# Optimization experiments

Hardware: AMD Instinct MI355X
Metric: run time of the kernel (lower is better)

## Reference

```python
import jax, jax.numpy as jnp
import numpy as np

NUM_USER = 50000
NUM_ITEM = 50000
NUM_NODES = NUM_USER + NUM_ITEM
DIM_LATENT = 256
DIM_ID = 64
NUM_EDGES = 2_000_000


def setup_inputs() -> dict:
    key = jax.random.key(0)
    ks = jax.random.split(key, 16)
    xn = lambda k, shape, s: (jax.random.normal(k, shape, dtype=jnp.float32) * s)
    # xavier-normal-ish std for [in,out] weights
    def xavier(k, fan_in, fan_out):
        std = float(np.sqrt(2.0 / (fan_in + fan_out)))
        return jax.random.normal(k, (fan_in, fan_out), dtype=jnp.float32) * std
    edge_index = jax.random.randint(ks[0], (2, NUM_EDGES), 0, NUM_NODES, dtype=jnp.int64)
    return {
        "features": xn(ks[1], (NUM_ITEM, DIM_LATENT), 1.0),
        "id_embedding": xn(ks[2], (NUM_NODES, DIM_ID), 1.0),
        "preference": xn(ks[3], (NUM_USER, DIM_LATENT), 0.1),
        "W_gcn0": xavier(ks[4], DIM_LATENT, DIM_ID),
        "W_gcn1": xavier(ks[5], DIM_ID, DIM_ID),
        "lin_w0": xavier(ks[6], DIM_LATENT, DIM_ID),
        "lin_b0": jnp.zeros((DIM_ID,), jnp.float32),
        "lin_w1": xavier(ks[7], DIM_ID, DIM_ID),
        "lin_b1": jnp.zeros((DIM_ID,), jnp.float32),
        "g_w0": xavier(ks[8], DIM_ID, DIM_ID),
        "g_b0": jnp.zeros((DIM_ID,), jnp.float32),
        "g_w1": xavier(ks[9], DIM_ID, DIM_ID),
        "g_b1": jnp.zeros((DIM_ID,), jnp.float32),
        "edge_index": edge_index,
    }


def _gcn(x, W, row, col, norm):
    # H = scatter_add(row, (x W)[col] * norm)
    h = x @ W                                  # [N, out]
    msg = h[col] * norm[:, None]               # [E, out] gather + scale
    return jax.ops.segment_sum(msg, row, num_segments=NUM_NODES)


def reference(features, id_embedding, preference, W_gcn0, W_gcn1,
              lin_w0, lin_b0, lin_w1, lin_b1, g_w0, g_b0, g_w1, g_b1,
              edge_index):
    row, col = edge_index[0], edge_index[1]
    # degree normalization: deg from scatter_add of ones over row
    deg = jax.ops.segment_sum(jnp.ones((row.shape[0],), jnp.float32), row,
                              num_segments=NUM_NODES)
    deg = jnp.maximum(deg, 1.0)
    dis = deg ** -0.5
    norm = dis[row] * dis[col]                 # [E]

    x = jnp.concatenate([preference, features], axis=0)   # [N, dim_latent]
    x = x / jnp.maximum(jnp.linalg.norm(x, axis=1, keepdims=True), 1e-12)

    lrelu = jax.nn.leaky_relu  # slope 0.01, matches torch default
    for W_gcn, lin_w, lin_b, g_w, g_b in (
        (W_gcn0, lin_w0, lin_b0, g_w0, g_b0),
        (W_gcn1, lin_w1, lin_b1, g_w1, g_b1),
    ):
        h = lrelu(_gcn(x, W_gcn, row, col, norm))          # [N, dim_id]
        x_hat = lrelu(x @ lin_w + lin_b) + id_embedding    # has_id=True
        x = lrelu(h @ g_w + g_b + x_hat)                   # concate=False
    return x
```

## Files before the change

### kernel.cpp

```cpp
#include <hip/hip_runtime.h>

#define NUM_USER   50000
#define NUM_ITEM   50000
#define NUM_NODES  100000
#define DIM_LATENT 256
#define DIM_ID     64
#define NUM_EDGES  2000000
#define NBUCKET    391
#define BPB        4096
#define NCHUNK     489
#define HSTRIDE    392
#define MAXBKT     8192
#define ZROW       NUM_NODES

typedef __attribute__((ext_vector_type(8))) short bf8_t;
typedef __attribute__((ext_vector_type(4))) float f4_t;
typedef __attribute__((ext_vector_type(2))) float f2_t;

static __device__ __forceinline__ float lrelu(float x) {
    return x > 0.0f ? x : 0.01f * x;
}
static __device__ __forceinline__ unsigned short f2bf(float f) {
    unsigned u = __float_as_uint(f);
    u += 0x7fff + ((u >> 16) & 1);
    return (unsigned short)(u >> 16);
}
static __device__ __forceinline__ unsigned cvtpk_bf16(float lo, float hi) {
    unsigned r;
    asm("v_cvt_pk_bf16_f32 %0, %1, %2" : "=v"(r) : "v"(lo), "v"(hi));
    return r;
}
static __device__ __forceinline__ float bf2f(unsigned short u) {
    return __uint_as_float(((unsigned)u) << 16);
}
static __device__ __forceinline__ float bflo(unsigned u) {
    return __uint_as_float(u << 16);
}
static __device__ __forceinline__ float bfhi(unsigned u) {
    return __uint_as_float(u & 0xffff0000u);
}
static __device__ __forceinline__ f2_t shfl2(f2_t v, int off) {
    long long l = __shfl_xor(__builtin_bit_cast(long long, v), off);
    return __builtin_bit_cast(f2_t, l);
}

__global__ void __launch_bounds__(256) k_hist(const int* __restrict__ row,
                                              int* __restrict__ hist) {
    __shared__ int lh[NBUCKET];
    const int g = blockIdx.x, t = threadIdx.x;
    for (int i = t; i < NBUCKET; i += 256) lh[i] = 0;
    __syncthreads();
    const int base = g * BPB;
    for (int i = 0; i < BPB; i += 256) {
        int e = base + i + t;
        if (e < NUM_EDGES) atomicAdd(&lh[row[e] >> 8], 1);
    }
    __syncthreads();
    for (int i = t; i < NBUCKET; i += 256) hist[g * HSTRIDE + i] = lh[i];
}

__global__ void __launch_bounds__(512) k_off1(int* __restrict__ hist,
                                              int* __restrict__ bcnt) {
    __shared__ int wsum[8];
    const int b = blockIdx.x, t = threadIdx.x;
    const int lane = t & 63, w = t >> 6;
    int c = (t < NCHUNK) ? hist[t * HSTRIDE + b] : 0;
    int v = c;
    #pragma unroll
    for (int off = 1; off < 64; off <<= 1) {
        int u = __shfl_up(v, off);
        if (lane >= off) v += u;
    }
    if (lane == 63) wsum[w] = v;
    __syncthreads();
    int add = 0;
    #pragma unroll
    for (int i = 0; i < 8; ++i) if (i < w) add += wsum[i];
    int incl = v + add;
    if (t < NCHUNK) hist[t * HSTRIDE + b] = incl - c;
    if (t == 511) bcnt[b] = incl;
}

__global__ void __launch_bounds__(512) k_bscan(const int* __restrict__ bcnt,
                                               int* __restrict__ boff) {
    __shared__ int wsum[8];
    const int t = threadIdx.x;
    const int lane = t & 63, w = t >> 6;
    int c = (t < NBUCKET) ? bcnt[t] : 0;
    int v = c;
    #pragma unroll
    for (int off = 1; off < 64; off <<= 1) {
        int u = __shfl_up(v, off);
        if (lane >= off) v += u;
    }
    if (lane == 63) wsum[w] = v;
    __syncthreads();
    int add = 0;
    #pragma unroll
    for (int i = 0; i < 8; ++i) if (i < w) add += wsum[i];
    int ex = v + add - c;
    if (t < NBUCKET) boff[t] = ex;
    if (t == NBUCKET - 1) boff[NBUCKET] = ex + c;
}

__global__ void __launch_bounds__(256) k_bin2(const int* __restrict__ row,
                                              const int* __restrict__ col,
                                              const int* __restrict__ hist,
                                              const int* __restrict__ boff,
                                              unsigned* __restrict__ epk) {
    __shared__ int curs[NBUCKET];
    const int g = blockIdx.x, t = threadIdx.x;
    for (int i = t; i < NBUCKET; i += 256) curs[i] = boff[i] + hist[g * HSTRIDE + i];
    __syncthreads();
    const int base = g * BPB;
    for (int i = 0; i < BPB; i += 256) {
        int e = base + i + t;
        if (e < NUM_EDGES) {
            int r = row[e];
            int pos = atomicAdd(&curs[r >> 8], 1);
            epk[pos] = ((unsigned)(r & 255) << 24) | (unsigned)col[e];
        }
    }
}

__global__ void __launch_bounds__(512) k_csr(unsigned* __restrict__ epk,
                                             const int* __restrict__ boff,
                                             int* __restrict__ offs,
                                             int* __restrict__ cnt,
                                             float* __restrict__ dis) {
    __shared__ unsigned stage[MAXBKT];
    __shared__ int lcnt[256];
    __shared__ int lofs[256];
    __shared__ int wsum[4];
    const int b = blockIdx.x, t = threadIdx.x;
    const int start = boff[b];
    int m = boff[b + 1] - start;
    if (m > MAXBKT) m = MAXBKT;

    if (t < 256) lcnt[t] = 0;
    for (int e = t; e < m; e += 512) stage[e] = epk[start + e];
    __syncthreads();
    for (int e = t; e < m; e += 512) atomicAdd(&lcnt[stage[e] >> 24], 1);
    __syncthreads();

    const int lane = t & 63, w = t >> 6;
    int c = (t < 256) ? lcnt[t] : 0;
    int v = c;
    #pragma unroll
    for (int off = 1; off < 64; off <<= 1) {
        int u = __shfl_up(v, off);
        if (lane >= off) v += u;
    }
    if (t < 256 && lane == 63) wsum[w] = v;
    __syncthreads();
    if (t < 256) {
        int add = 0;
        #pragma unroll
        for (int i = 0; i < 4; ++i) if (i < w) add += wsum[i];
        int ex = v + add - c;
        lofs[t] = start + ex;
        int n = (b << 8) + t;
        if (n < NUM_NODES) {
            offs[n] = start + ex;
            cnt[n]  = c;
            dis[n]  = rsqrtf((float)max(c, 1));
        }
    }
    __syncthreads();
    for (int e = t; e < m; e += 512) {
        unsigned p = stage[e];
        int pos = atomicAdd(&lofs[p >> 24], 1);
        epk[pos] = p & 0x00ffffffu;
    }
}

__global__ void __launch_bounds__(256) k_wprep(const float* __restrict__ Wg,
                                               const float* __restrict__ Wl,
                                               unsigned short* __restrict__ wfrag,
                                               unsigned* __restrict__ hbf8z) {
    if (blockIdx.x == 0 && threadIdx.x < 16)
        hbf8z[(size_t)ZROW * 16 + threadIdx.x] = 0u;
    int g = blockIdx.x * 256 + threadIdx.x;
    if (g >= 4096) return;
    int ks = g >> 9;
    int t  = (g >> 6) & 7;
    int l  = g & 63;
    const float* W = (t < 4) ? Wg : Wl;
    int colg = (t & 3) * 16 + (l & 15);
    int kb = ks * 32 + (l >> 4) * 8;
    unsigned short o[8];
    #pragma unroll
    for (int e = 0; e < 8; ++e) o[e] = f2bf(W[(size_t)(kb + e) * DIM_ID + colg]);
    unsigned short* dst = wfrag + (size_t)g * 8;
    #pragma unroll
    for (int e = 0; e < 8; ++e) dst[e] = o[e];
}

__global__ void __launch_bounds__(256) k_wprep64(const float* __restrict__ W0,
                                                 const float* __restrict__ W1,
                                                 const float* __restrict__ W2,
                                                 const float* __restrict__ W3,
                                                 unsigned short* __restrict__ frag) {
    int g = blockIdx.x * 256 + threadIdx.x;
    if (g >= 2048) return;
    int m = g >> 9;
    int r = g & 511;
    int ks = r >> 8;
    int t  = (r >> 6) & 3;
    int l  = r & 63;
    const float* W = (m == 0) ? W0 : (m == 1) ? W1 : (m == 2) ? W2 : W3;
    int colg = t * 16 + (l & 15);
    int kb = ks * 32 + (l >> 4) * 8;
    unsigned short o[8];
    #pragma unroll
    for (int e = 0; e < 8; ++e) o[e] = f2bf(W[(size_t)(kb + e) * DIM_ID + colg]);
    unsigned short* dst = frag + (size_t)g * 8;
    #pragma unroll
    for (int e = 0; e < 8; ++e) dst[e] = o[e];
}

__global__ void __launch_bounds__(256, 3) k_l1(
    const float* __restrict__ pref, const float* __restrict__ feat,
    const unsigned short* __restrict__ wfrag,
    const float* __restrict__ lb,   const float* __restrict__ idemb,
    const float* __restrict__ dis,
    unsigned char* __restrict__ hbf8, unsigned short* __restrict__ xhat)
{
    __shared__ unsigned short st[4][16][68];
    const int lane = threadIdx.x & 63;
    const int w = threadIdx.x >> 6;
    const int ql = lane & 15, q = lane >> 4;
    const int rowBase = (blockIdx.x * 4 + w) * 16;
    const int rown = rowBase + ql;
    const int rc = (rown < NUM_NODES) ? rown : 0;
    const float* src = (rc < NUM_USER) ? (pref + (size_t)rc * DIM_LATENT)
                                       : (feat + (size_t)(rc - NUM_USER) * DIM_LATENT);

    bf8_t af[8];
    float ss = 0.0f;
    #pragma unroll
    for (int ks = 0; ks < 8; ++ks) {
        float4 va = *reinterpret_cast<const float4*>(src + ks * 32 + q * 8);
        float4 vb = *reinterpret_cast<const float4*>(src + ks * 32 + q * 8 + 4);
        ss += va.x*va.x + va.y*va.y + va.z*va.z + va.w*va.w
            + vb.x*vb.x + vb.y*vb.y + vb.z*vb.z + vb.w*vb.w;
        uint4 au;
        au.x = cvtpk_bf16(va.x, va.y);
        au.y = cvtpk_bf16(va.z, va.w);
        au.z = cvtpk_bf16(vb.x, vb.y);
        au.w = cvtpk_bf16(vb.z, vb.w);
        af[ks] = __builtin_bit_cast(bf8_t, au);
    }
    ss += __shfl_xor(ss, 16);
    ss += __shfl_xor(ss, 32);
    float rn = 1.0f / fmaxf(sqrtf(ss), 1e-12f);

    f4_t acc[8];
    #pragma unroll
    for (int t = 0; t < 8; ++t) acc[t] = (f4_t){0.f, 0.f, 0.f, 0.f};

    const bf8_t* wf = reinterpret_cast<const bf8_t*>(wfrag);
    #pragma unroll
    for (int ks = 0; ks < 8; ++ks) {
        #pragma unroll
        for (int t = 0; t < 8; ++t) {
            bf8_t b = wf[(ks * 8 + t) * 64 + lane];
            acc[t] = __builtin_amdgcn_mfma_f32_16x16x32_bf16(af[ks], b, acc[t], 0, 0, 0);
        }
    }

    float rn4[4];
    #pragma unroll
    for (int reg = 0; reg < 4; ++reg) rn4[reg] = __shfl(rn, q * 4 + reg);

    int nn[4];
    float dn[4];
    #pragma unroll
    for (int reg = 0; reg < 4; ++reg) {
        nn[reg] = rowBase + q * 4 + reg;
        dn[reg] = (nn[reg] < NUM_NODES) ? dis[nn[reg]] * rn4[reg] : 0.0f;
    }

    #pragma unroll
    for (int t = 0; t < 4; ++t)
        #pragma unroll
        for (int reg = 0; reg < 4; ++reg)
            st[w][q * 4 + reg][t * 16 + ql] = f2bf(acc[t][reg] * dn[reg]);
    #pragma unroll
    for (int it = 0; it < 4; ++it) {
        int i = it * 64 + lane;
        int r = i >> 4, c8 = i & 15;
        int n = rowBase + r;
        uint2 s = *reinterpret_cast<const uint2*>(&st[w][r][c8 * 4]);
        if (n < NUM_NODES) {
            int p = __builtin_amdgcn_cvt_pk_fp8_f32(bflo(s.x), bfhi(s.x), 0, false);
            p = __builtin_amdgcn_cvt_pk_fp8_f32(bflo(s.y), bfhi(s.y), p, true);
            *reinterpret_cast<unsigned*>(hbf8 + (size_t)n * DIM_ID + c8 * 4) = (unsigned)p;
        }
    }

    #pragma unroll
    for (int t = 4; t < 8; ++t) {
        int colg = (t - 4) * 16 + ql;
        float lbl = lb[colg];
        #pragma unroll
        for (int reg = 0; reg < 4; ++reg)
            st[w][q * 4 + reg][colg] = f2bf(lrelu(acc[t][reg] * rn4[reg] + lbl));
    }
    #pragma unroll
    for (int it = 0; it < 4; ++it) {
        int i = it * 64 + lane;
        int r = i >> 4, c8 = i & 15;
        int n = rowBase + r;
        if (n < NUM_NODES) {
            uint2 s = *reinterpret_cast<const uint2*>(&st[w][r][c8 * 4]);
            float4 idv = *reinterpret_cast<const float4*>(&idemb[(size_t)n * DIM_ID + c8 * 4]);
            uint2 o;
            o.x = cvtpk_bf16(bflo(s.x) + idv.x, bfhi(s.x) + idv.y);
            o.y = cvtpk_bf16(bflo(s.y) + idv.z, bfhi(s.y) + idv.w);
            *reinterpret_cast<uint2*>(&xhat[(size_t)n * DIM_ID + c8 * 4]) = o;
        }
    }
}

__global__ void __launch_bounds__(256, 8) k_gather(
    const unsigned char* __restrict__ hbf8, const float* __restrict__ dis,
    const int* __restrict__ offs, const int* __restrict__ cnt,
    const int* __restrict__ ecol, unsigned short* __restrict__ Hb)
{
    const int w = threadIdx.x >> 6;
    const int lane = threadIdx.x & 63;
    const int g = lane >> 3;
    const int k = lane & 7;
    const int n = blockIdx.x * 4 + w;

    const float dn = dis[n];
    const int start = offs[n];
    const int m = cnt[n];

    f2_t s01 = {0.f, 0.f}, s23 = {0.f, 0.f}, s45 = {0.f, 0.f}, s67 = {0.f, 0.f};

    for (int base = 0; base < m; base += 64) {
        int e = base + lane;
        int ec = (e < m) ? ecol[start + e] : ZROW;
        int lim = m - base; if (lim > 64) lim = 64;
        int ns = (lim + 31) >> 5;
        for (int s = 0; s < ns; ++s) {
            int i0 = s * 32 + g;
            int c0 = __shfl(ec, i0);
            int c1 = __shfl(ec, i0 + 8);
            int c2 = __shfl(ec, i0 + 16);
            int c3 = __shfl(ec, i0 + 24);
            uint2 u0 = *reinterpret_cast<const uint2*>(hbf8 + (size_t)(c0 << 6) + (k << 3));
            uint2 u1 = *reinterpret_cast<const uint2*>(hbf8 + (size_t)(c1 << 6) + (k << 3));
            uint2 u2 = *reinterpret_cast<const uint2*>(hbf8 + (size_t)(c2 << 6) + (k << 3));
            uint2 u3 = *reinterpret_cast<const uint2*>(hbf8 + (size_t)(c3 << 6) + (k << 3));
            s01 += __builtin_amdgcn_cvt_pk_f32_fp8(u0.x, false);
            s23 += __builtin_amdgcn_cvt_pk_f32_fp8(u0.x, true);
            s45 += __builtin_amdgcn_cvt_pk_f32_fp8(u0.y, false);
            s67 += __builtin_amdgcn_cvt_pk_f32_fp8(u0.y, true);
            s01 += __builtin_amdgcn_cvt_pk_f32_fp8(u1.x, false);
            s23 += __builtin_amdgcn_cvt_pk_f32_fp8(u1.x, true);
            s45 += __builtin_amdgcn_cvt_pk_f32_fp8(u1.y, false);
            s67 += __builtin_amdgcn_cvt_pk_f32_fp8(u1.y, true);
            s01 += __builtin_amdgcn_cvt_pk_f32_fp8(u2.x, false);
            s23 += __builtin_amdgcn_cvt_pk_f32_fp8(u2.x, true);
            s45 += __builtin_amdgcn_cvt_pk_f32_fp8(u2.y, false);
            s67 += __builtin_amdgcn_cvt_pk_f32_fp8(u2.y, true);
            s01 += __builtin_amdgcn_cvt_pk_f32_fp8(u3.x, false);
            s23 += __builtin_amdgcn_cvt_pk_f32_fp8(u3.x, true);
            s45 += __builtin_amdgcn_cvt_pk_f32_fp8(u3.y, false);
            s67 += __builtin_amdgcn_cvt_pk_f32_fp8(u3.y, true);
        }
    }
    #pragma unroll
    for (int off = 8; off <= 32; off <<= 1) {
        s01 += shfl2(s01, off);
        s23 += shfl2(s23, off);
        s45 += shfl2(s45, off);
        s67 += shfl2(s67, off);
    }
    if (lane < 8) {
        uint4 o;
        o.x = cvtpk_bf16(s01.x * dn, s01.y * dn);
        o.y = cvtpk_bf16(s23.x * dn, s23.y * dn);
        o.z = cvtpk_bf16(s45.x * dn, s45.y * dn);
        o.w = cvtpk_bf16(s67.x * dn, s67.y * dn);
        *reinterpret_cast<uint4*>(&Hb[(size_t)n * DIM_ID + lane * 8]) = o;
    }
}

__global__ void __launch_bounds__(256, 3) k_mid(
    const unsigned short* __restrict__ Hb, const unsigned short* __restrict__ xhat1,
    const unsigned short* __restrict__ wf64,
    const float* __restrict__ gb,  const float* __restrict__ lb1,
    const float* __restrict__ idemb, const float* __restrict__ dis,
    unsigned char* __restrict__ hbf8, unsigned short* __restrict__ xhat2)
{
    __shared__ unsigned short x1s[4][16][DIM_ID];
    __shared__ unsigned short st[4][16][68];
    const int lane = threadIdx.x & 63;
    const int w = threadIdx.x >> 6;
    const int ql = lane & 15, q = lane >> 4;
    const int rowBase = (blockIdx.x * 4 + w) * 16;
    const int rowc = min(rowBase + ql, NUM_NODES - 1);

    bf8_t ha[2];
    #pragma unroll
    for (int ks = 0; ks < 2; ++ks) {
        uint4 u = *reinterpret_cast<const uint4*>(&Hb[(size_t)rowc * DIM_ID + ks * 32 + q * 8]);
        bf8_t a;
        a[0] = (short)f2bf(lrelu(bflo(u.x))); a[1] = (short)f2bf(lrelu(bfhi(u.x)));
        a[2] = (short)f2bf(lrelu(bflo(u.y))); a[3] = (short)f2bf(lrelu(bfhi(u.y)));
        a[4] = (short)f2bf(lrelu(bflo(u.z))); a[5] = (short)f2bf(lrelu(bfhi(u.z)));
        a[6] = (short)f2bf(lrelu(bflo(u.w))); a[7] = (short)f2bf(lrelu(bfhi(u.w)));
        ha[ks] = a;
    }

    const bf8_t* gw0f = reinterpret_cast<const bf8_t*>(wf64);
    f4_t acc1[4];
    #pragma unroll
    for (int t = 0; t < 4; ++t) acc1[t] = (f4_t){0.f, 0.f, 0.f, 0.f};
    #pragma unroll
    for (int ks = 0; ks < 2; ++ks)
        #pragma unroll
        for (int t = 0; t < 4; ++t)
            acc1[t] = __builtin_amdgcn_mfma_f32_16x16x32_bf16(ha[ks], gw0f[(ks * 4 + t) * 64 + lane], acc1[t], 0, 0, 0);

    int nn[4];
    #pragma unroll
    for (int reg = 0; reg < 4; ++reg) nn[reg] = rowBase + q * 4 + reg;

    #pragma unroll
    for (int t = 0; t < 4; ++t) {
        int colg = t * 16 + ql;
        float gbl = gb[colg];
        #pragma unroll
        for (int reg = 0; reg < 4; ++reg) {
            float xh = bf2f(xhat1[(size_t)min(nn[reg], NUM_NODES - 1) * DIM_ID + colg]);
            x1s[w][q * 4 + reg][colg] = f2bf(lrelu(acc1[t][reg] + gbl + xh));
        }
    }
    __syncthreads();

    bf8_t xa[2];
    #pragma unroll
    for (int ks = 0; ks < 2; ++ks)
        xa[ks] = *reinterpret_cast<const bf8_t*>(&x1s[w][ql][ks * 32 + q * 8]);

    const bf8_t* wg1f = reinterpret_cast<const bf8_t*>(wf64 + 512 * 8);
    const bf8_t* lw1f = reinterpret_cast<const bf8_t*>(wf64 + 1024 * 8);
    f4_t acc2[8];
    #pragma unroll
    for (int t = 0; t < 8; ++t) acc2[t] = (f4_t){0.f, 0.f, 0.f, 0.f};
    #pragma unroll
    for (int ks = 0; ks < 2; ++ks) {
        #pragma unroll
        for (int t = 0; t < 4; ++t)
            acc2[t] = __builtin_amdgcn_mfma_f32_16x16x32_bf16(xa[ks], wg1f[(ks * 4 + t) * 64 + lane], acc2[t], 0, 0, 0);
        #pragma unroll
        for (int t = 0; t < 4; ++t)
            acc2[4 + t] = __builtin_amdgcn_mfma_f32_16x16x32_bf16(xa[ks], lw1f[(ks * 4 + t) * 64 + lane], acc2[4 + t], 0, 0, 0);
    }

    float dn[4];
    #pragma unroll
    for (int reg = 0; reg < 4; ++reg)
        dn[reg] = (nn[reg] < NUM_NODES) ? dis[nn[reg]] : 0.0f;

    #pragma unroll
    for (int t = 0; t < 4; ++t)
        #pragma unroll
        for (int reg = 0; reg < 4; ++reg)
            st[w][q * 4 + reg][t * 16 + ql] = f2bf(acc2[t][reg] * dn[reg]);
    #pragma unroll
    for (int it = 0; it < 4; ++it) {
        int i = it * 64 + lane;
        int r = i >> 4, c8 = i & 15;
        int n = rowBase + r;
        uint2 s = *reinterpret_cast<const uint2*>(&st[w][r][c8 * 4]);
        if (n < NUM_NODES) {
            int p = __builtin_amdgcn_cvt_pk_fp8_f32(bflo(s.x), bfhi(s.x), 0, false);
            p = __builtin_amdgcn_cvt_pk_fp8_f32(bflo(s.y), bfhi(s.y), p, true);
            *reinterpret_cast<unsigned*>(hbf8 + (size_t)n * DIM_ID + c8 * 4) = (unsigned)p;
        }
    }

    #pragma unroll
    for (int t = 0; t < 4; ++t) {
        int colg = t * 16 + ql;
        float lbl = lb1[colg];
        #pragma unroll
        for (int reg = 0; reg < 4; ++reg)
            st[w][q * 4 + reg][colg] = f2bf(lrelu(acc2[4 + t][reg] + lbl));
    }
    #pragma unroll
    for (int it = 0; it < 4; ++it) {
        int i = it * 64 + lane;
        int r = i >> 4, c8 = i & 15;
        int n = rowBase + r;
        if (n < NUM_NODES) {
            uint2 s = *reinterpret_cast<const uint2*>(&st[w][r][c8 * 4]);
            float4 idv = *reinterpret_cast<const float4*>(&idemb[(size_t)n * DIM_ID + c8 * 4]);
            uint2 o;
            o.x = cvtpk_bf16(bflo(s.x) + idv.x, bfhi(s.x) + idv.y);
            o.y = cvtpk_bf16(bflo(s.y) + idv.z, bfhi(s.y) + idv.w);
            *reinterpret_cast<uint2*>(&xhat2[(size_t)n * DIM_ID + c8 * 4]) = o;
        }
    }
}

__global__ void __launch_bounds__(256, 3) k_final(
    const unsigned short* __restrict__ Hb, const unsigned short* __restrict__ xhat,
    const unsigned short* __restrict__ wf64,
    const float* __restrict__ gb, float* __restrict__ out)
{
    const int lane = threadIdx.x & 63;
    const int w = threadIdx.x >> 6;
    const int ql = lane & 15, q = lane >> 4;
    const int rowBase = (blockIdx.x * 4 + w) * 16;
    const int rowc = min(rowBase + ql, NUM_NODES - 1);

    bf8_t ha[2];
    #pragma unroll
    for (int ks = 0; ks < 2; ++ks) {
        uint4 u = *reinterpret_cast<const uint4*>(&Hb[(size_t)rowc * DIM_ID + ks * 32 + q * 8]);
        bf8_t a;
        a[0] = (short)f2bf(lrelu(bflo(u.x))); a[1] = (short)f2bf(lrelu(bfhi(u.x)));
        a[2] = (short)f2bf(lrelu(bflo(u.y))); a[3] = (short)f2bf(lrelu(bfhi(u.y)));
        a[4] = (short)f2bf(lrelu(bflo(u.z))); a[5] = (short)f2bf(lrelu(bfhi(u.z)));
        a[6] = (short)f2bf(lrelu(bflo(u.w))); a[7] = (short)f2bf(lrelu(bfhi(u.w)));
        ha[ks] = a;
    }

    const bf8_t* gw1f = reinterpret_cast<const bf8_t*>(wf64 + 1536 * 8);
    f4_t acc[4];
    #pragma unroll
    for (int t = 0; t < 4; ++t) acc[t] = (f4_t){0.f, 0.f, 0.f, 0.f};
    #pragma unroll
    for (int ks = 0; ks < 2; ++ks)
        #pragma unroll
        for (int t = 0; t < 4; ++t)
            acc[t] = __builtin_amdgcn_mfma_f32_16x16x32_bf16(ha[ks], gw1f[(ks * 4 + t) * 64 + lane], acc[t], 0, 0, 0);

    int nn[4];
    #pragma unroll
    for (int reg = 0; reg < 4; ++reg) nn[reg] = rowBase + q * 4 + reg;

    #pragma unroll
    for (int t = 0; t < 4; ++t) {
        int colg = t * 16 + ql;
        float gbl = gb[colg];
        #pragma unroll
        for (int reg = 0; reg < 4; ++reg)
            if (nn[reg] < NUM_NODES) {
                size_t o = (size_t)nn[reg] * DIM_ID + colg;
                out[o] = lrelu(acc[t][reg] + gbl + bf2f(xhat[o]));
            }
    }
}

extern "C" void kernel_launch(void* const* d_in, const int* in_sizes, int n_in,
                              void* d_out, int out_size, void* d_ws, size_t ws_size,
                              hipStream_t stream)
{
    const float* features = (const float*)d_in[0];
    const float* idemb    = (const float*)d_in[1];
    const float* pref     = (const float*)d_in[2];
    const float* Wg0      = (const float*)d_in[3];
    const float* Wg1      = (const float*)d_in[4];
    const float* lw0      = (const float*)d_in[5];
    const float* lb0      = (const float*)d_in[6];
    const float* lw1      = (const float*)d_in[7];
    const float* lb1      = (const float*)d_in[8];
    const float* gw0      = (const float*)d_in[9];
    const float* gb0      = (const float*)d_in[10];
    const float* gw1      = (const float*)d_in[11];
    const float* gb1      = (const float*)d_in[12];
    const int*   edges    = (const int*)d_in[13];
    const int*   row      = edges;
    const int*   col      = edges + NUM_EDGES;

    char* ws = (char*)d_ws;
    int*      hist  = (int*)(ws + 0);
    int*      bcnt  = (int*)(ws + 1048576);
    int*      boff  = (int*)(ws + 1052672);
    int*      offs  = (int*)(ws + 1056768);
    int*      cnt   = (int*)(ws + 1581056);
    float*    dis   = (float*)(ws + 2105344);
    unsigned short* wfrag = (unsigned short*)(ws + 2629632);
    unsigned short* wf64  = (unsigned short*)(ws + 2695168);
    unsigned short* Hbf = (unsigned short*)(ws + 20000000);
    unsigned* epk  = (unsigned*)(ws + 53960704);
    unsigned char*  hbf8  = (unsigned char*)(ws + 62349312);
    unsigned short* xhatb = (unsigned short*)(ws + 68749376);
    float* out   = (float*)d_out;

    const int l1Blocks = (NUM_NODES + 63) / 64;
    const int gatherBlocks = NUM_NODES / 4;

    k_wprep<<<16, 256, 0, stream>>>(Wg0, lw0, wfrag, (unsigned*)hbf8);
    k_wprep64<<<8, 256, 0, stream>>>(gw0, Wg1, lw1, gw1, wf64);

    k_hist<<<NCHUNK, 256, 0, stream>>>(row, hist);
    k_off1<<<NBUCKET, 512, 0, stream>>>(hist, bcnt);
    k_bscan<<<1, 512, 0, stream>>>(bcnt, boff);
    k_bin2<<<NCHUNK, 256, 0, stream>>>(row, col, hist, boff, epk);
    k_csr<<<NBUCKET, 512, 0, stream>>>(epk, boff, offs, cnt, dis);

    k_l1<<<l1Blocks, 256, 0, stream>>>(pref, features, wfrag, lb0, idemb, dis,
                                       hbf8, xhatb);

    k_gather<<<gatherBlocks, 256, 0, stream>>>(hbf8, dis, offs, cnt, (const int*)epk, Hbf);

    k_mid<<<l1Blocks, 256, 0, stream>>>(Hbf, xhatb, wf64, gb0, lb1, idemb, dis,
                                        hbf8, xhatb);

    k_gather<<<gatherBlocks, 256, 0, stream>>>(hbf8, dis, offs, cnt, (const int*)epk, Hbf);
    k_final<<<l1Blocks, 256, 0, stream>>>(Hbf, xhatb, wf64, gb1, out);
}
```

Before: 197.4 us.

## Split k_l1 K-dimension across four waves with LDS reduction per 16-row tile

```diff
diff --git a/kernel.cpp b/kernel.cpp
--- a/kernel.cpp
+++ b/kernel.cpp
@@ -219,41 +219,47 @@
     for (int e = 0; e < 8; ++e) dst[e] = o[e];
 }
 
-__global__ void __launch_bounds__(256, 3) k_l1(
+__global__ void __launch_bounds__(256, 4) k_l1(
     const float* __restrict__ pref, const float* __restrict__ feat,
     const unsigned short* __restrict__ wfrag,
     const float* __restrict__ lb,   const float* __restrict__ idemb,
     const float* __restrict__ dis,
     unsigned char* __restrict__ hbf8, unsigned short* __restrict__ xhat)
 {
-    __shared__ unsigned short st[4][16][68];
-    const int lane = threadIdx.x & 63;
-    const int w = threadIdx.x >> 6;
+    __shared__ float accw[4][32][64];
+    __shared__ float ssb[4][16];
+    __shared__ unsigned short stA[16][68];
+    __shared__ unsigned short stB[16][68];
+    const int t256 = threadIdx.x;
+    const int lane = t256 & 63;
+    const int w = t256 >> 6;
     const int ql = lane & 15, q = lane >> 4;
-    const int rowBase = (blockIdx.x * 4 + w) * 16;
+    const int rowBase = blockIdx.x * 16;
     const int rown = rowBase + ql;
-    const int rc = (rown < NUM_NODES) ? rown : 0;
-    const float* src = (rc < NUM_USER) ? (pref + (size_t)rc * DIM_LATENT)
-                                       : (feat + (size_t)(rc - NUM_USER) * DIM_LATENT);
-
-    bf8_t af[8];
-    float ss = 0.0f;
-    #pragma unroll
-    for (int ks = 0; ks < 8; ++ks) {
-        float4 va = *reinterpret_cast<const float4*>(src + ks * 32 + q * 8);
-        float4 vb = *reinterpret_cast<const float4*>(src + ks * 32 + q * 8 + 4);
-        ss += va.x*va.x + va.y*va.y + va.z*va.z + va.w*va.w
-            + vb.x*vb.x + vb.y*vb.y + vb.z*vb.z + vb.w*vb.w;
-        uint4 au;
-        au.x = cvtpk_bf16(va.x, va.y);
-        au.y = cvtpk_bf16(va.z, va.w);
-        au.z = cvtpk_bf16(vb.x, vb.y);
-        au.w = cvtpk_bf16(vb.z, vb.w);
-        af[ks] = __builtin_bit_cast(bf8_t, au);
-    }
+    const float* src = (rown < NUM_USER) ? (pref + (size_t)rown * DIM_LATENT)
+                                         : (feat + (size_t)(rown - NUM_USER) * DIM_LATENT);
+    const int ks0 = 2 * w;
+
+    float4 v0 = *reinterpret_cast<const float4*>(src + ks0 * 32 + q * 8);
+    float4 v1 = *reinterpret_cast<const float4*>(src + ks0 * 32 + q * 8 + 4);
+    float4 v2 = *reinterpret_cast<const float4*>(src + (ks0 + 1) * 32 + q * 8);
+    float4 v3 = *reinterpret_cast<const float4*>(src + (ks0 + 1) * 32 + q * 8 + 4);
+
+    float ss = v0.x*v0.x + v0.y*v0.y + v0.z*v0.z + v0.w*v0.w
+             + v1.x*v1.x + v1.y*v1.y + v1.z*v1.z + v1.w*v1.w
+             + v2.x*v2.x + v2.y*v2.y + v2.z*v2.z + v2.w*v2.w
+             + v3.x*v3.x + v3.y*v3.y + v3.z*v3.z + v3.w*v3.w;
     ss += __shfl_xor(ss, 16);
     ss += __shfl_xor(ss, 32);
-    float rn = 1.0f / fmaxf(sqrtf(ss), 1e-12f);
+    if (lane < 16) ssb[w][lane] = ss;
+
+    uint4 au0, au1;
+    au0.x = cvtpk_bf16(v0.x, v0.y); au0.y = cvtpk_bf16(v0.z, v0.w);
+    au0.z = cvtpk_bf16(v1.x, v1.y); au0.w = cvtpk_bf16(v1.z, v1.w);
+    au1.x = cvtpk_bf16(v2.x, v2.y); au1.y = cvtpk_bf16(v2.z, v2.w);
+    au1.z = cvtpk_bf16(v3.x, v3.y); au1.w = cvtpk_bf16(v3.z, v3.w);
+    bf8_t a0 = __builtin_bit_cast(bf8_t, au0);
+    bf8_t a1 = __builtin_bit_cast(bf8_t, au1);
 
     f4_t acc[8];
     #pragma unroll
@@ -261,65 +267,69 @@
 
     const bf8_t* wf = reinterpret_cast<const bf8_t*>(wfrag);
     #pragma unroll
-    for (int ks = 0; ks < 8; ++ks) {
-        #pragma unroll
-        for (int t = 0; t < 8; ++t) {
-            bf8_t b = wf[(ks * 8 + t) * 64 + lane];
-            acc[t] = __builtin_amdgcn_mfma_f32_16x16x32_bf16(af[ks], b, acc[t], 0, 0, 0);
+    for (int t = 0; t < 8; ++t)
+        acc[t] = __builtin_amdgcn_mfma_f32_16x16x32_bf16(a0, wf[(ks0 * 8 + t) * 64 + lane], acc[t], 0, 0, 0);
+    #pragma unroll
+    for (int t = 0; t < 8; ++t)
+        acc[t] = __builtin_amdgcn_mfma_f32_16x16x32_bf16(a1, wf[((ks0 + 1) * 8 + t) * 64 + lane], acc[t], 0, 0, 0);
+
+    #pragma unroll
+    for (int t = 0; t < 8; ++t)
+        #pragma unroll
+        for (int reg = 0; reg < 4; ++reg)
+            accw[w][t * 4 + reg][lane] = acc[t][reg];
+    __syncthreads();
+
+    float rnl[4];
+    #pragma unroll
+    for (int reg = 0; reg < 4; ++reg) {
+        int r = q * 4 + reg;
+        float s = (ssb[0][r] + ssb[1][r]) + (ssb[2][r] + ssb[3][r]);
+        rnl[reg] = 1.0f / fmaxf(sqrtf(s), 1e-12f);
+    }
+
+    #pragma unroll
+    for (int j = 0; j < 2; ++j) {
+        int t = ks0 + j;
+        float av[4];
+        #pragma unroll
+        for (int reg = 0; reg < 4; ++reg)
+            av[reg] = (accw[0][t * 4 + reg][lane] + accw[1][t * 4 + reg][lane])
+                    + (accw[2][t * 4 + reg][lane] + accw[3][t * 4 + reg][lane]);
+        if (t < 4) {
+            int colg = t * 16 + ql;
+            #pragma unroll
+            for (int reg = 0; reg < 4; ++reg) {
+                float dn = dis[rowBase + q * 4 + reg] * rnl[reg];
+                stA[q * 4 + reg][colg] = f2bf(av[reg] * dn);
+            }
+        } else {
+            int colg = (t - 4) * 16 + ql;
+            float lbl = lb[colg];
+            #pragma unroll
+            for (int reg = 0; reg < 4; ++reg)
+                stB[q * 4 + reg][colg] = f2bf(lrelu(av[reg] * rnl[reg] + lbl));
         }
     }
-
-    float rn4[4];
-    #pragma unroll
-    for (int reg = 0; reg < 4; ++reg) rn4[reg] = __shfl(rn, q * 4 + reg);
-
-    int nn[4];
-    float dn[4];
-    #pragma unroll
-    for (int reg = 0; reg < 4; ++reg) {
-        nn[reg] = rowBase + q * 4 + reg;
-        dn[reg] = (nn[reg] < NUM_NODES) ? dis[nn[reg]] * rn4[reg] : 0.0f;
-    }
-
-    #pragma unroll
-    for (int t = 0; t < 4; ++t)
-        #pragma unroll
-        for (int reg = 0; reg < 4; ++reg)
-            st[w][q * 4 + reg][t * 16 + ql] = f2bf(acc[t][reg] * dn[reg]);
-    #pragma unroll
-    for (int it = 0; it < 4; ++it) {
-        int i = it * 64 + lane;
-        int r = i >> 4, c8 = i & 15;
+    __syncthreads();
+
+    {
+        int r = t256 >> 4, c8 = t256 & 15;
         int n = rowBase + r;
-        uint2 s = *reinterpret_cast<const uint2*>(&st[w][r][c8 * 4]);
-        if (n < NUM_NODES) {
-            int p = __builtin_amdgcn_cvt_pk_fp8_f32(bflo(s.x), bfhi(s.x), 0, false);
-            p = __builtin_amdgcn_cvt_pk_fp8_f32(bflo(s.y), bfhi(s.y), p, true);
-            *reinterpret_cast<unsigned*>(hbf8 + (size_t)n * DIM_ID + c8 * 4) = (unsigned)p;
-        }
-    }
-
-    #pragma unroll
-    for (int t = 4; t < 8; ++t) {
-        int colg = (t - 4) * 16 + ql;
-        float lbl = lb[colg];
-        #pragma unroll
-        for (int reg = 0; reg < 4; ++reg)
-            st[w][q * 4 + reg][colg] = f2bf(lrelu(acc[t][reg] * rn4[reg] + lbl));
-    }
-    #pragma unroll
-    for (int it = 0; it < 4; ++it) {
-        int i = it * 64 + lane;
-        int r = i >> 4, c8 = i & 15;
+        uint2 s = *reinterpret_cast<const uint2*>(&stA[r][c8 * 4]);
+        int p = __builtin_amdgcn_cvt_pk_fp8_f32(bflo(s.x), bfhi(s.x), 0, false);
+        p = __builtin_amdgcn_cvt_pk_fp8_f32(bflo(s.y), bfhi(s.y), p, true);
+        *reinterpret_cast<unsigned*>(hbf8 + (size_t)n * DIM_ID + c8 * 4) = (unsigned)p;
+    }
+    {
+        int r = t256 >> 4, c8 = t256 & 15;
         int n = rowBase + r;
-        if (n < NUM_NODES) {
-            uint2 s = *reinterpret_cast<const uint2*>(&st[w][r][c8 * 4]);
-            float4 idv = *reinterpret_cast<const float4*>(&idemb[(size_t)n * DIM_ID + c8 * 4]);
-            uint2 o;
-            o.x = cvtpk_bf16(bflo(s.x) + idv.x, bfhi(s.x) + idv.y);
-            o.y = cvtpk_bf16(bflo(s.y) + idv.z, bfhi(s.y) + idv.w);
-            *reinterpret_cast<uint2*>(&xhat[(size_t)n * DIM_ID + c8 * 4]) = o;
-        }
+        uint2 s = *reinterpret_cast<const uint2*>(&stB[r][c8 * 4]);
+        float4 idv = *reinterpret_cast<const float4*>(&idemb[(size_t)n * DIM_ID + c8 * 4]);
+        uint2 o;
+        o.x = cvtpk_bf16(bflo(s.x) + idv.x, bfhi(s.x) + idv.y);
+        o.y = cvtpk_bf16(bflo(s.y) + idv.z, bfhi(s.y) + idv.w);
+        *reinterpret_cast<uint2*>(&xhat[(size_t)n * DIM_ID + c8 * 4]) = o;
     }
 }
 
@@ -596,7 +606,8 @@
     unsigned short* xhatb = (unsigned short*)(ws + 68749376);
     float* out   = (float*)d_out;
 
-    const int l1Blocks = (NUM_NODES + 63) / 64;
+    const int l1Blocks = NUM_NODES / 16;
+    const int midBlocks = (NUM_NODES + 63) / 64;
     const int gatherBlocks = NUM_NODES / 4;
 
     k_wprep<<<16, 256, 0, stream>>>(Wg0, lw0, wfrag, (unsigned*)hbf8);
@@ -613,9 +624,9 @@
 
     k_gather<<<gatherBlocks, 256, 0, stream>>>(hbf8, dis, offs, cnt, (const int*)epk, Hbf);
 
-    k_mid<<<l1Blocks, 256, 0, stream>>>(Hbf, xhatb, wf64, gb0, lb1, idemb, dis,
-                                        hbf8, xhatb);
+    k_mid<<<midBlocks, 256, 0, stream>>>(Hbf, xhatb, wf64, gb0, lb1, idemb, dis,
+                                         hbf8, xhatb);
 
     k_gather<<<gatherBlocks, 256, 0, stream>>>(hbf8, dis, offs, cnt, (const int*)epk, Hbf);
-    k_final<<<l1Blocks, 256, 0, stream>>>(Hbf, xhatb, wf64, gb1, out);
-}
+    k_final<<<midBlocks, 256, 0, stream>>>(Hbf, xhatb, wf64, gb1, out);
+}
```

Result: no change. 195.4 us, median of 2 (-1.0%).
